# Optimization experiments

Measured on AMD Instinct MI355X. Metric: run time of the kernel, lower is better.

Reference implementation:

```python
import jax, jax.numpy as jnp
import numpy as np

HIDDEN = 512
TEXT_DIM = 768
NUM_HEADS = 8
NUM_GROUPS = 32
GN_EPS = 1e-5
COS_EPS = 1e-6


def setup_inputs() -> dict:
    key = jax.random.key(0)
    ks = jax.random.split(key, 9)
    s = 0.02
    return {
        "x": jax.random.normal(ks[0], (16, HIDDEN, 64, 64), jnp.float32),
        "text_emb": jax.random.normal(ks[1], (16, 77, TEXT_DIM), jnp.float32),
        "gn_weight": jnp.ones((HIDDEN,), jnp.float32),
        "gn_bias": jnp.zeros((HIDDEN,), jnp.float32),
        "Wq": jax.random.normal(ks[2], (HIDDEN, HIDDEN), jnp.float32) * s,
        "Wk": jax.random.normal(ks[3], (HIDDEN, TEXT_DIM), jnp.float32) * s,
        "Wv": jax.random.normal(ks[4], (HIDDEN, TEXT_DIM), jnp.float32) * s,
        "Wo": jax.random.normal(ks[5], (HIDDEN, HIDDEN), jnp.float32) * s,
        "bo": jnp.zeros((HIDDEN,), jnp.float32),
    }


def reference(x, text_emb, gn_weight, gn_bias, Wq, Wk, Wv, Wo, bo):
    B, C, H, W = x.shape
    N_img = H * W
    nh, hd = NUM_HEADS, C // NUM_HEADS

    # GroupNorm(32, C): normalize over (channels-in-group, H, W)
    xg = x.reshape(B, NUM_GROUPS, -1)
    mu = xg.mean(axis=-1, keepdims=True)
    var = jnp.mean(jnp.square(xg - mu), axis=-1, keepdims=True)
    xn = ((xg - mu) * jax.lax.rsqrt(var + GN_EPS)).reshape(B, C, H, W)
    xn = xn * gn_weight[None, :, None, None] + gn_bias[None, :, None, None]

    x_flat = xn.reshape(B, C, N_img).transpose(0, 2, 1)  # [B, N_img, C]

    q = jnp.einsum('bnc,dc->bnd', x_flat, Wq)            # [B, N_img, C]
    k = jnp.einsum('btc,dc->btd', text_emb, Wk)          # [B, N_text, C]
    v = jnp.einsum('btc,dc->btd', text_emb, Wv)

    # split heads -> [B, nh, N, hd]
    q = q.reshape(B, N_img, nh, hd).transpose(0, 2, 1, 3)
    k = k.reshape(B, -1, nh, hd).transpose(0, 2, 1, 3)
    v = v.reshape(B, -1, nh, hd).transpose(0, 2, 1, 3)

    # cosine-sim attention: L2-normalize q and k, scale = 1.0
    q = q / (jnp.linalg.norm(q, axis=-1, keepdims=True) + COS_EPS)
    k = k / (jnp.linalg.norm(k, axis=-1, keepdims=True) + COS_EPS)

    scores = jnp.einsum('bhqd,bhkd->bhqk', q, k)         # [B, nh, N_img, N_text]
    attn = jax.nn.softmax(scores, axis=-1)
    out = jnp.einsum('bhqk,bhkd->bhqd', attn, v)         # [B, nh, N_img, hd]

    out = out.transpose(0, 2, 1, 3).reshape(B, N_img, C)
    out = jnp.einsum('bnc,dc->bnd', out, Wo) + bo
    out = out.transpose(0, 2, 1).reshape(B, C, H, W)
    return x + out
```

## Files before the change

### kernel.cpp

```cpp
#include <hip/hip_runtime.h>
#include <math.h>


typedef unsigned short u16;
typedef __attribute__((ext_vector_type(8))) __bf16 bf16x8;
typedef __attribute__((ext_vector_type(4))) float f32x4;

typedef __attribute__((address_space(1))) unsigned int as1_u32;
typedef __attribute__((address_space(3))) unsigned int as3_u32;

__device__ __forceinline__ float b2f(u16 u) {
  union { unsigned int i; float f; } c; c.i = ((unsigned int)u) << 16; return c.f;
}
__device__ __forceinline__ u16 f2b(float f) {
  union { float f; unsigned int i; } c; c.f = f;
  unsigned int i = c.i + 0x7fffu + ((c.i >> 16) & 1u);
  return (u16)(i >> 16);
}

__device__ __forceinline__ void g2lds16(const void* g, void* l) {
  __builtin_amdgcn_global_load_lds((const as1_u32*)g, (as3_u32*)l, 16, 0, 0);
}

__global__ void k_castall(const float* __restrict__ Wq, const float* __restrict__ Wk,
                          const float* __restrict__ Wv, const float* __restrict__ Wo,
                          const float* __restrict__ text,
                          u16* __restrict__ wq_b, u16* __restrict__ wkv_b,
                          u16* __restrict__ wo_b, u16* __restrict__ text_b) {
  const int i = blockIdx.x * 256 + threadIdx.x, st = gridDim.x * 256;
  for (int j = i; j < 262144; j += st) wq_b[j] = f2b(Wq[j]);
  for (int j = i; j < 393216; j += st) wkv_b[j] = f2b(Wk[j]);
  for (int j = i; j < 393216; j += st) wkv_b[393216 + j] = f2b(Wv[j]);
  for (int j = i; j < 262144; j += st) wo_b[j] = f2b(Wo[j]);
  for (int j = i; j < 946176; j += st) text_b[j] = f2b(text[j]);
}

__global__ __launch_bounds__(256) void k_gnstats(const float* __restrict__ x,
                                                 float* __restrict__ stats) {
  int bg = blockIdx.x;
  const float4* p = (const float4*)(x + (size_t)bg * 65536);
  float s = 0.f, ss = 0.f;
  for (int i = threadIdx.x; i < 16384; i += 256) {
    float4 v = p[i];
    s  += v.x + v.y + v.z + v.w;
    ss += v.x*v.x + v.y*v.y + v.z*v.z + v.w*v.w;
  }
  for (int o = 1; o < 64; o <<= 1) { s += __shfl_xor(s, o, 64); ss += __shfl_xor(ss, o, 64); }
  __shared__ float as_[4], bs_[4];
  int w = threadIdx.x >> 6;
  if ((threadIdx.x & 63) == 0) { as_[w] = s; bs_[w] = ss; }
  __syncthreads();
  if (threadIdx.x == 0) {
    s  = as_[0] + as_[1] + as_[2] + as_[3];
    ss = bs_[0] + bs_[1] + bs_[2] + bs_[3];
    float mu  = s * (1.f / 65536.f);
    float var = ss * (1.f / 65536.f) - mu * mu;
    stats[2*bg]   = mu;
    stats[2*bg+1] = rsqrtf(var + 1e-5f);
  }
}

__global__ __launch_bounds__(256, 2) void k_qproj(
    const float* __restrict__ x, const float* __restrict__ stats,
    const float* __restrict__ gw, const float* __restrict__ gb,
    const u16* __restrict__ Wqb, u16* __restrict__ qb) {
  __shared__ u16 Al[128 * 64];
  __shared__ u16 Bl[256 * 64];
  __shared__ float cw[512], cb[512];
  const int tid = threadIdx.x;
  const int o = blockIdx.x;
  const int mi = ((o >> 4) << 3) + (o & 7);
  const int ni = (o >> 3) & 1;
  const int m0 = mi << 7, n0 = ni << 8;
  const int b = m0 >> 12, hw0 = m0 & 4095;

  for (int c = tid; c < 512; c += 256) {
    const int g = (b << 5) + (c >> 4);
    const float mu = stats[2*g], rs = stats[2*g+1];
    const float wg = gw[c] * rs;
    cw[c] = wg; cb[c] = gb[c] - mu * wg;
  }

  const int l = tid & 63, w = tid >> 6;
  const int wm = (w & 1) << 6;
  const int wn = (w >> 1) << 7;
  const int lr = l & 15, lg = l >> 4;

  f32x4 acc[4][8];
#pragma unroll
  for (int i = 0; i < 4; ++i)
#pragma unroll
    for (int j = 0; j < 8; ++j) acc[i][j] = {0.f, 0.f, 0.f, 0.f};

  const int rl = l >> 3, slot = l & 7;
  const int c8 = (slot ^ rl) << 3;
  int brow[8];
#pragma unroll
  for (int j = 0; j < 8; ++j) brow[j] = n0 + (w << 6) + (j << 3) + rl;

  const int tokl = tid & 127;
  const int chg = tid >> 7;
  const float* xb = x + (((size_t)b) << 9) * 4096;
  __syncthreads();

  for (int ks = 0; ks < 8; ++ks) {
#pragma unroll
    for (int j = 0; j < 8; ++j)
      g2lds16(Wqb + (size_t)brow[j] * 512 + (ks << 6) + c8,
              Bl + (((w << 6) + (j << 3)) << 6));
#pragma unroll
    for (int jj = 0; jj < 8; ++jj) {
      const int ch4 = (((chg << 3) + jj) << 2);
      const int c = (ks << 6) + ch4;
      const float v0 = xb[(size_t)(c + 0) * 4096 + hw0 + tokl];
      const float v1 = xb[(size_t)(c + 1) * 4096 + hw0 + tokl];
      const float v2 = xb[(size_t)(c + 2) * 4096 + hw0 + tokl];
      const float v3 = xb[(size_t)(c + 3) * 4096 + hw0 + tokl];
      union { __bf16 h[4]; ushort4 u; } pk;
      pk.h[0] = (__bf16)(v0 * cw[c + 0] + cb[c + 0]);
      pk.h[1] = (__bf16)(v1 * cw[c + 1] + cb[c + 1]);
      pk.h[2] = (__bf16)(v2 * cw[c + 2] + cb[c + 2]);
      pk.h[3] = (__bf16)(v3 * cw[c + 3] + cb[c + 3]);
      const int sl = (((ch4 >> 3) ^ (tokl & 7)) << 3) + (ch4 & 7);
      *(ushort4*)(Al + (tokl << 6) + sl) = pk.u;
    }
    __syncthreads();
    bf16x8 af[4][2];
#pragma unroll
    for (int i = 0; i < 4; ++i) {
      const int ar = wm + i * 16 + lr;
      af[i][0] = *(const bf16x8*)(Al + (ar << 6) + (((lg    ) ^ (ar & 7)) << 3));
      af[i][1] = *(const bf16x8*)(Al + (ar << 6) + (((lg + 4) ^ (ar & 7)) << 3));
    }
#pragma unroll
    for (int j = 0; j < 8; ++j) {
      const int br = wn + j * 16 + lr;
      const bf16x8 b0 = *(const bf16x8*)(Bl + (br << 6) + (((lg    ) ^ (br & 7)) << 3));
      const bf16x8 b1 = *(const bf16x8*)(Bl + (br << 6) + (((lg + 4) ^ (br & 7)) << 3));
#pragma unroll
      for (int i = 0; i < 4; ++i) {
        acc[i][j] = __builtin_amdgcn_mfma_f32_16x16x32_bf16(af[i][0], b0, acc[i][j], 0, 0, 0);
        acc[i][j] = __builtin_amdgcn_mfma_f32_16x16x32_bf16(af[i][1], b1, acc[i][j], 0, 0, 0);
      }
    }
    __syncthreads();
  }

  const int lg4 = lg << 2;
#pragma unroll
  for (int i = 0; i < 4; ++i) {
#pragma unroll
    for (int r = 0; r < 4; ++r) {
      const int row = m0 + wm + i * 16 + lg4 + r;
#pragma unroll
      for (int h2 = 0; h2 < 2; ++h2) {
        float ss = 0.f;
#pragma unroll
        for (int j = h2 * 4; j < h2 * 4 + 4; ++j) {
          const float v = acc[i][j][r]; ss += v * v;
        }
        ss += __shfl_xor(ss, 1, 64); ss += __shfl_xor(ss, 2, 64);
        ss += __shfl_xor(ss, 4, 64); ss += __shfl_xor(ss, 8, 64);
        const float sc = 1.f / (sqrtf(ss) + 1e-6f);
#pragma unroll
        for (int j = h2 * 4; j < h2 * 4 + 4; ++j)
          qb[(size_t)row * 512 + n0 + wn + j * 16 + lr] = f2b(acc[i][j][r] * sc);
      }
    }
  }
}

template <int MODE>
__global__ __launch_bounds__(256) void k_gemm(
    const u16* __restrict__ A, const u16* __restrict__ BT,
    int M, int N, int K,
    float* __restrict__ outf,
    const float* __restrict__ xres, const float* __restrict__ bias) {
  __shared__ u16 Al[128 * 64];
  __shared__ u16 Bl[128 * 64];
  const int tid = threadIdx.x;
  const int l = tid & 63, w = tid >> 6;

  const int nwg = gridDim.x * gridDim.y;
  int lin = blockIdx.y * gridDim.x + blockIdx.x;
  lin = (lin & 7) * (nwg >> 3) + (lin >> 3);
  const int m0 = (lin / gridDim.x) << 7, n0 = (lin % gridDim.x) << 7;

  const int wm = (w >> 1) << 6, wn = (w & 1) << 6;
  const int lr = l & 15, lg = l >> 4;

  f32x4 acc[4][4];
#pragma unroll
  for (int i = 0; i < 4; ++i)
#pragma unroll
    for (int j = 0; j < 4; ++j) acc[i][j] = {0.f, 0.f, 0.f, 0.f};

  const int rl = l >> 3, slot = l & 7;
  const int c8 = (slot ^ rl) << 3;
  int arow[4], brow[4];
#pragma unroll
  for (int j = 0; j < 4; ++j) {
    const int r_local = (w << 5) + (j << 3) + rl;
    arow[j] = min(m0 + r_local, M - 1);
    brow[j] = n0 + r_local;
  }

  const int ksteps = K >> 6;
  for (int ks = 0; ks < ksteps; ++ks) {
    const int kb = (ks << 6) + c8;
#pragma unroll
    for (int j = 0; j < 4; ++j)
      g2lds16(A + (size_t)arow[j] * K + kb, Al + (((w << 5) + (j << 3)) << 6));
#pragma unroll
    for (int j = 0; j < 4; ++j)
      g2lds16(BT + (size_t)brow[j] * K + kb, Bl + (((w << 5) + (j << 3)) << 6));
    __syncthreads();
    bf16x8 bfr[4][2];
#pragma unroll
    for (int j = 0; j < 4; ++j) {
      const int br = wn + j * 16 + lr;
      bfr[j][0] = *(const bf16x8*)(Bl + (br << 6) + (((lg    ) ^ (br & 7)) << 3));
      bfr[j][1] = *(const bf16x8*)(Bl + (br << 6) + (((lg + 4) ^ (br & 7)) << 3));
    }
#pragma unroll
    for (int i = 0; i < 4; ++i) {
      const int ar = wm + i * 16 + lr;
      const bf16x8 a0 = *(const bf16x8*)(Al + (ar << 6) + (((lg    ) ^ (ar & 7)) << 3));
      const bf16x8 a1 = *(const bf16x8*)(Al + (ar << 6) + (((lg + 4) ^ (ar & 7)) << 3));
#pragma unroll
      for (int j = 0; j < 4; ++j) {
        acc[i][j] = __builtin_amdgcn_mfma_f32_16x16x32_bf16(a0, bfr[j][0], acc[i][j], 0, 0, 0);
        acc[i][j] = __builtin_amdgcn_mfma_f32_16x16x32_bf16(a1, bfr[j][1], acc[i][j], 0, 0, 0);
      }
    }
    __syncthreads();
  }

  const int lg4 = lg << 2;
#pragma unroll
  for (int i = 0; i < 4; ++i) {
#pragma unroll
    for (int j = 0; j < 4; ++j) {
#pragma unroll
      for (int r = 0; r < 4; ++r) {
        const int row = m0 + wm + i * 16 + lg4 + r;
        const int col = n0 + wn + j * 16 + lr;
        const float v = acc[i][j][r];
        if (MODE == 0) {
          if (row < M) outf[(size_t)row * N + col] = v;
        } else {
          const int bb = col >> 12, hw = col & 4095;
          const size_t o = (((size_t)bb << 9) + row) * 4096 + hw;
          outf[o] = xres[o] + bias[row] + v;
        }
      }
    }
  }
}

__global__ __launch_bounds__(64) void k_kvnorm(const float* __restrict__ kv,
                                               u16* __restrict__ kn,
                                               u16* __restrict__ vn) {
  const int row = blockIdx.x;
  const int h = blockIdx.y;
  const int d = threadIdx.x;
  const int b = row / 77, t = row - b * 77;
  const float kx = kv[(size_t)row * 1024 + h * 64 + d];
  float ss = kx * kx;
  for (int o = 1; o < 64; o <<= 1) ss += __shfl_xor(ss, o, 64);
  const float sc = 1.f / (sqrtf(ss) + 1e-6f);
  const size_t ob = (((size_t)(b * 8 + h)) * 77 + t) * 64 + d;
  kn[ob] = f2b(kx * sc);
  vn[ob] = f2b(kv[(size_t)row * 1024 + 512 + h * 64 + d]);
}

__global__ __launch_bounds__(256) void k_attn2(
    const u16* __restrict__ q, const u16* __restrict__ kn,
    const u16* __restrict__ vn, u16* __restrict__ out) {
  __shared__ u16 Kl[96 * 72];
  __shared__ u16 Vt[64 * 104];
  __shared__ u16 Pl[64 * 104];
  const int qt = blockIdx.x, h = blockIdx.y, b = blockIdx.z;
  const size_t kvb = ((size_t)(b * 8 + h)) * (77 * 64);
  const int tid = threadIdx.x;
  for (int u = tid; u < 768; u += 256) {
    const int row = u >> 3, c8v = (u & 7) << 3;
    uint4 v = make_uint4(0, 0, 0, 0);
    if (row < 77) v = *(const uint4*)(kn + kvb + row * 64 + c8v);
    *(uint4*)(Kl + row * 72 + c8v) = v;
  }
  for (int u = tid; u < 768; u += 256) {
    const int row = u >> 3, c8v = (u & 7) << 3;
    uint4 v = make_uint4(0, 0, 0, 0);
    if (row < 77) v = *(const uint4*)(vn + kvb + row * 64 + c8v);
    const u16* pv = (const u16*)&v;
#pragma unroll
    for (int j = 0; j < 8; ++j) Vt[(c8v + j) * 104 + row] = pv[j];
  }
  __syncthreads();
  const int l = tid & 63, w = tid >> 6;
  const int lr = l & 15, lg = l >> 4;

  const int qrow = (b << 12) + (qt << 6) + (w << 4) + lr;
  bf16x8 af0 = *(const bf16x8*)(q + (size_t)qrow * 512 + h * 64 + lg * 8);
  bf16x8 af1 = *(const bf16x8*)(q + (size_t)qrow * 512 + h * 64 + 32 + lg * 8);
  f32x4 s[6];
#pragma unroll
  for (int nt = 0; nt < 6; ++nt) {
    s[nt] = {0.f, 0.f, 0.f, 0.f};
    bf16x8 bk0 = *(const bf16x8*)(Kl + (nt * 16 + lr) * 72 + lg * 8);
    bf16x8 bk1 = *(const bf16x8*)(Kl + (nt * 16 + lr) * 72 + 32 + lg * 8);
    s[nt] = __builtin_amdgcn_mfma_f32_16x16x32_bf16(af0, bk0, s[nt], 0, 0, 0);
    s[nt] = __builtin_amdgcn_mfma_f32_16x16x32_bf16(af1, bk1, s[nt], 0, 0, 0);
  }
#pragma unroll
  for (int r = 0; r < 4; ++r) {
    if (lr >= 13) s[4][r] = -1e30f;
    s[5][r] = -1e30f;
  }
#pragma unroll
  for (int r = 0; r < 4; ++r) {
    float m = s[0][r];
#pragma unroll
    for (int nt = 1; nt < 6; ++nt) m = fmaxf(m, s[nt][r]);
    m = fmaxf(m, __shfl_xor(m, 1, 64)); m = fmaxf(m, __shfl_xor(m, 2, 64));
    m = fmaxf(m, __shfl_xor(m, 4, 64)); m = fmaxf(m, __shfl_xor(m, 8, 64));
    float sum = 0.f;
#pragma unroll
    for (int nt = 0; nt < 6; ++nt) { s[nt][r] = __expf(s[nt][r] - m); sum += s[nt][r]; }
    sum += __shfl_xor(sum, 1, 64); sum += __shfl_xor(sum, 2, 64);
    sum += __shfl_xor(sum, 4, 64); sum += __shfl_xor(sum, 8, 64);
    const float inv = 1.f / sum;
    const int qlocal = (w << 4) + (lg << 2) + r;
#pragma unroll
    for (int nt = 0; nt < 6; ++nt)
      Pl[qlocal * 104 + nt * 16 + lr] = f2b(s[nt][r] * inv);
  }
  __syncthreads();

  bf16x8 pa0 = *(const bf16x8*)(Pl + ((w << 4) + lr) * 104 + lg * 8);
  bf16x8 pa1 = *(const bf16x8*)(Pl + ((w << 4) + lr) * 104 + 32 + lg * 8);
  bf16x8 pa2 = *(const bf16x8*)(Pl + ((w << 4) + lr) * 104 + 64 + lg * 8);
  f32x4 o[4];
#pragma unroll
  for (int nt = 0; nt < 4; ++nt) {
    o[nt] = {0.f, 0.f, 0.f, 0.f};
    bf16x8 bv0 = *(const bf16x8*)(Vt + (nt * 16 + lr) * 104 + lg * 8);
    bf16x8 bv1 = *(const bf16x8*)(Vt + (nt * 16 + lr) * 104 + 32 + lg * 8);
    bf16x8 bv2 = *(const bf16x8*)(Vt + (nt * 16 + lr) * 104 + 64 + lg * 8);
    o[nt] = __builtin_amdgcn_mfma_f32_16x16x32_bf16(pa0, bv0, o[nt], 0, 0, 0);
    o[nt] = __builtin_amdgcn_mfma_f32_16x16x32_bf16(pa1, bv1, o[nt], 0, 0, 0);
    o[nt] = __builtin_amdgcn_mfma_f32_16x16x32_bf16(pa2, bv2, o[nt], 0, 0, 0);
  }
#pragma unroll
  for (int r = 0; r < 4; ++r) {
    const int n = (b << 12) + (qt << 6) + (w << 4) + (lg << 2) + r;
#pragma unroll
    for (int nt = 0; nt < 4; ++nt)
      out[(size_t)n * 512 + h * 64 + nt * 16 + lr] = f2b(o[nt][r]);
  }
}

extern "C" void kernel_launch(void* const* d_in, const int* in_sizes, int n_in,
                              void* d_out, int out_size, void* d_ws, size_t ws_size,
                              hipStream_t stream) {
  (void)in_sizes; (void)n_in; (void)out_size; (void)ws_size;
  const float* x    = (const float*)d_in[0];
  const float* text = (const float*)d_in[1];
  const float* gnw  = (const float*)d_in[2];
  const float* gnb  = (const float*)d_in[3];
  const float* Wq   = (const float*)d_in[4];
  const float* Wk   = (const float*)d_in[5];
  const float* Wv   = (const float*)d_in[6];
  const float* Wo   = (const float*)d_in[7];
  const float* bo   = (const float*)d_in[8];
  float* out = (float*)d_out;

  char* ws = (char*)d_ws;
  size_t off = 0;
  auto alloc = [&](size_t bytes) -> void* {
    void* p = ws + off; off += (bytes + 255) & ~(size_t)255; return p;
  };
  float* stats = (float*)alloc(512 * 2 * 4);
  u16* wq_b    = (u16*)alloc((size_t)512 * 512 * 2);
  u16* wkv_b   = (u16*)alloc((size_t)1024 * 768 * 2);
  u16* wo_b    = (u16*)alloc((size_t)512 * 512 * 2);
  u16* text_b  = (u16*)alloc((size_t)1232 * 768 * 2);
  float* kv_f  = (float*)alloc((size_t)1232 * 1024 * 4);
  u16* kn      = (u16*)alloc((size_t)16 * 8 * 77 * 64 * 2);
  u16* vn      = (u16*)alloc((size_t)16 * 8 * 77 * 64 * 2);
  u16* ao      = (u16*)alloc((size_t)65536 * 512 * 2);
  u16* qb      = (u16*)alloc((size_t)65536 * 512 * 2);

  k_castall<<<dim3(512), 256, 0, stream>>>(Wq, Wk, Wv, Wo, text,
                                           wq_b, wkv_b, wo_b, text_b);

  k_gnstats<<<dim3(512), 256, 0, stream>>>(x, stats);

  k_gemm<0><<<dim3(8, 10), 256, 0, stream>>>(text_b, wkv_b, 1232, 1024, 768,
                                             kv_f, nullptr, nullptr);
  k_kvnorm<<<dim3(1232, 8), 64, 0, stream>>>(kv_f, kn, vn);

  k_qproj<<<dim3(1024), 256, 0, stream>>>(x, stats, gnw, gnb, wq_b, qb);

  k_attn2<<<dim3(64, 8, 16), 256, 0, stream>>>(qb, kn, vn, ao);

  k_gemm<2><<<dim3(512, 4), 256, 0, stream>>>(wo_b, ao, 512, 65536, 512,
                                              out, x, bo);
}
```

Baseline: 297.1 us.

## Double-buffer normalized activation tile and read Wq fragments directly from global

In the fused GroupNorm+Q-projection GEMM, the activation tile becomes double-buffered in LDS. The next k-slice's normalize-and-cast now overlaps the MFMA work on the current slice. The Wq B-operand is no longer staged through LDS; each wave loads its bf16x8 fragments straight from global memory, relying on L2/L1 since the weight is small and shared across blocks. This cuts LDS usage and one barrier per iteration, but puts global-load latency in the MFMA loop and may add redundant weight traffic.

New measurement: 331.9 us. 1.12x slower.

```diff
diff --git a/kernel.cpp b/kernel.cpp
--- a/kernel.cpp
+++ b/kernel.cpp
@@ -64,8 +64,7 @@
     const float* __restrict__ x, const float* __restrict__ stats,
     const float* __restrict__ gw, const float* __restrict__ gb,
     const u16* __restrict__ Wqb, u16* __restrict__ qb) {
-  __shared__ u16 Al[128 * 64];
-  __shared__ u16 Bl[256 * 64];
+  __shared__ u16 Al[2][128 * 64];
   __shared__ float cw[512], cb[512];
   const int tid = threadIdx.x;
   const int o = blockIdx.x;
@@ -92,22 +91,11 @@
 #pragma unroll
     for (int j = 0; j < 8; ++j) acc[i][j] = {0.f, 0.f, 0.f, 0.f};
 
-  const int rl = l >> 3, slot = l & 7;
-  const int c8 = (slot ^ rl) << 3;
-  int brow[8];
-#pragma unroll
-  for (int j = 0; j < 8; ++j) brow[j] = n0 + (w << 6) + (j << 3) + rl;
-
   const int tokl = tid & 127;
   const int chg = tid >> 7;
   const float* xb = x + (((size_t)b) << 9) * 4096;
-  __syncthreads();
-
-  for (int ks = 0; ks < 8; ++ks) {
-#pragma unroll
-    for (int j = 0; j < 8; ++j)
-      g2lds16(Wqb + (size_t)brow[j] * 512 + (ks << 6) + c8,
-              Bl + (((w << 6) + (j << 3)) << 6));
+
+  auto stageA = [&](int ks, u16* dst) {
 #pragma unroll
     for (int jj = 0; jj < 8; ++jj) {
       const int ch4 = (((chg << 3) + jj) << 2);
@@ -122,21 +110,30 @@
       pk.h[2] = (__bf16)(v2 * cw[c + 2] + cb[c + 2]);
       pk.h[3] = (__bf16)(v3 * cw[c + 3] + cb[c + 3]);
       const int sl = (((ch4 >> 3) ^ (tokl & 7)) << 3) + (ch4 & 7);
-      *(ushort4*)(Al + (tokl << 6) + sl) = pk.u;
-    }
-    __syncthreads();
+      *(ushort4*)(dst + (tokl << 6) + sl) = pk.u;
+    }
+  };
+
+  __syncthreads();
+  stageA(0, Al[0]);
+  __syncthreads();
+
+  for (int ks = 0; ks < 8; ++ks) {
+    const u16* Ac = Al[ks & 1];
+    if (ks + 1 < 8) stageA(ks + 1, Al[(ks + 1) & 1]);
     bf16x8 af[4][2];
 #pragma unroll
     for (int i = 0; i < 4; ++i) {
       const int ar = wm + i * 16 + lr;
-      af[i][0] = *(const bf16x8*)(Al + (ar << 6) + (((lg    ) ^ (ar & 7)) << 3));
-      af[i][1] = *(const bf16x8*)(Al + (ar << 6) + (((lg + 4) ^ (ar & 7)) << 3));
+      af[i][0] = *(const bf16x8*)(Ac + (ar << 6) + (((lg    ) ^ (ar & 7)) << 3));
+      af[i][1] = *(const bf16x8*)(Ac + (ar << 6) + (((lg + 4) ^ (ar & 7)) << 3));
     }
 #pragma unroll
     for (int j = 0; j < 8; ++j) {
-      const int br = wn + j * 16 + lr;
-      const bf16x8 b0 = *(const bf16x8*)(Bl + (br << 6) + (((lg    ) ^ (br & 7)) << 3));
-      const bf16x8 b1 = *(const bf16x8*)(Bl + (br << 6) + (((lg + 4) ^ (br & 7)) << 3));
+      const int br = n0 + wn + j * 16 + lr;
+      const u16* wrow = Wqb + (size_t)br * 512 + (ks << 6);
+      const bf16x8 b0 = *(const bf16x8*)(wrow + lg * 8);
+      const bf16x8 b1 = *(const bf16x8*)(wrow + 32 + lg * 8);
 #pragma unroll
       for (int i = 0; i < 4; ++i) {
         acc[i][j] = __builtin_amdgcn_mfma_f32_16x16x32_bf16(af[i][0], b0, acc[i][j], 0, 0, 0);
@@ -250,8 +247,8 @@
           if (row < M) outf[(size_t)row * N + col] = v;
         } else {
           const int bb = col >> 12, hw = col & 4095;
-          const size_t o = (((size_t)bb << 9) + row) * 4096 + hw;
-          outf[o] = xres[o] + bias[row] + v;
+          const size_t oo = (((size_t)bb << 9) + row) * 4096 + hw;
+          outf[oo] = xres[oo] + bias[row] + v;
         }
       }
     }
```
